# Performance work log

Measured on AMD Instinct MI355X. Metric: run time of the kernel, lower is better.

The kernel has to match this reference:

```python
import jax, jax.numpy as jnp
import numpy as np

B, DIM = 8192, 4096

def setup_inputs() -> dict:
    key = jax.random.key(0)
    k1, k2 = jax.random.split(key)
    a = jax.random.normal(k1, (B, 1, DIM), dtype=jnp.float32)
    b = jax.random.normal(k2, (B, 1, DIM), dtype=jnp.float32)
    return {"a": a, "b": b}

def reference(a, b):
    # Original layer builds a circulant matrix from b: row i is roll(b, shift=i),
    # i.e. C[i, k] = b[(k - i) % dim], then computes out[k] = sum_i a[i] * C[i, k]
    # = circular convolution of a and b. Equivalent (and O(d log d)) via FFT:
    d = a.shape[-1]
    fa = jnp.fft.rfft(a.astype(jnp.float32), axis=-1)
    fb = jnp.fft.rfft(b.astype(jnp.float32), axis=-1)
    out = jnp.fft.irfft(fa * fb, n=d, axis=-1)  # (B, 1, dim)
    return out.astype(a.dtype)
```

## Files before the change

kernel.cpp:

```cpp
#include <hip/hip_runtime.h>

#define FFT_N 4096
#define NT    256
#define SK(i) ((i) + ((i) >> 4))
#define PM(m) ((((m) & 3) << 2) | ((m) >> 2))

typedef float    cplx __attribute__((ext_vector_type(2)));
typedef _Float16 h4   __attribute__((ext_vector_type(4)));

__device__ __forceinline__ cplx mkc(float re, float im) { cplx c; c.x = re; c.y = im; return c; }
__device__ __forceinline__ h4 packh(cplx a, cplx b) {
    h4 v; v.x = (_Float16)a.x; v.y = (_Float16)a.y; v.z = (_Float16)b.x; v.w = (_Float16)b.y;
    return v;
}
__device__ __forceinline__ cplx cmul(cplx a, cplx b) {
    return mkc(a.x * b.x - a.y * b.y, a.x * b.y + a.y * b.x);
}
__device__ __forceinline__ cplx cmulc(cplx a, cplx b) {
    return mkc(a.x * b.x + a.y * b.y, a.y * b.x - a.x * b.y);
}

template <int SGN, bool PERMIN>
__device__ __forceinline__ void ip16(cplx* x) {
    const float S = (float)SGN;
    const float C1 = 0.92387953251128675613f;
    const float S1 = 0.38268343236508977173f;
    const float R2 = 0.70710678118654752440f;
#define BF4(i0, i1, i2, i3) do { \
        cplx x0 = x[i0], x1 = x[i1], x2 = x[i2], x3 = x[i3]; \
        cplx t0 = x0 + x2, t1 = x0 - x2; \
        cplx t2 = x1 + x3, t3 = x1 - x3; \
        cplx it3 = mkc(-S * t3.y, S * t3.x); \
        x[i0] = t0 + t2; x[i1] = t1 + it3; \
        x[i2] = t0 - t2; x[i3] = t1 - it3; \
    } while (0)
    if (!PERMIN) { BF4(0, 4, 8, 12); BF4(1, 5, 9, 13); BF4(2, 6, 10, 14); BF4(3, 7, 11, 15); }
    else         { BF4(0, 1, 2, 3);  BF4(4, 5, 6, 7);  BF4(8, 9, 10, 11); BF4(12, 13, 14, 15); }
    const cplx w1 = mkc(C1, S * S1), w2 = mkc(R2, S * R2), w3 = mkc(S1, S * C1);
    const cplx w6 = mkc(-R2, S * R2), w9 = mkc(-C1, -S * S1);
    x[5]  = cmul(x[5],  w1);
    x[6]  = cmul(x[6],  w2);
    x[7]  = cmul(x[7],  w3);
    x[9]  = cmul(x[9],  w2);
    { cplx v = x[10]; x[10] = mkc(-S * v.y, S * v.x); }
    x[11] = cmul(x[11], w6);
    x[13] = cmul(x[13], w3);
    x[14] = cmul(x[14], w6);
    x[15] = cmul(x[15], w9);
    if (!PERMIN) { BF4(0, 1, 2, 3);  BF4(4, 5, 6, 7);  BF4(8, 9, 10, 11); BF4(12, 13, 14, 15); }
    else         { BF4(0, 4, 8, 12); BF4(1, 5, 9, 13); BF4(2, 6, 10, 14); BF4(3, 7, 11, 15); }
#undef BF4
}

__global__ void twiddle_init(cplx* __restrict__ twA, cplx* __restrict__ twB) {
    int m = blockIdx.x * NT + threadIdx.x;
    if (m >= 4352) return;
    float s, c;
    if (m < 4096) {
        int r = m >> 8, t = m & 255;
        sincosf(-6.28318530717958647692f * (float)(t * r) / 4096.0f, &s, &c);
        twA[m] = mkc(c, s);
    } else {
        int k = m - 4096;
        int r = k >> 4, j = k & 15;
        sincosf(-6.28318530717958647692f * (float)(j * r) / 256.0f, &s, &c);
        twB[k] = mkc(c, s);
    }
}

__global__ __launch_bounds__(NT) void circconv4096_kernel(
    const float* __restrict__ A, const float* __restrict__ Bv,
    float* __restrict__ O,
    const cplx* __restrict__ twA, const cplx* __restrict__ twB)
{
    __shared__ h4 Z[SK(4095) + 1];
    const int t = threadIdx.x;
    const size_t r0 = (size_t)blockIdx.x * 2;
    const float* a0 = A + r0 * FFT_N;
    const float* b0 = Bv + r0 * FFT_N;
    const float* a1 = a0 + FFT_N;
    const float* b1 = b0 + FFT_N;
    float* o0 = O + r0 * FFT_N;
    float* o1 = o0 + FFT_N;

    cplx x0[16], x1[16];

#pragma unroll
    for (int q = 0; q < 16; ++q) { int g = t + 256 * q; x0[q] = mkc(a0[g], b0[g]); }
#pragma unroll
    for (int q = 0; q < 16; ++q) { int g = t + 256 * q; x1[q] = mkc(a1[g], b1[g]); }
    ip16<-1, false>(x0);
    ip16<-1, false>(x1);
#pragma unroll
    for (int m = 1; m < 16; ++m) {
        cplx w = twA[PM(m) * 256 + t];
        x0[m] = cmul(x0[m], w);
        x1[m] = cmul(x1[m], w);
    }
#pragma unroll
    for (int m = 0; m < 16; ++m) Z[SK(t + 256 * PM(m))] = packh(x0[m], x1[m]);
    __syncthreads();

    const int j = t & 15;
    const int base = ((t >> 4) << 8) + j;

#pragma unroll
    for (int q = 0; q < 16; ++q) {
        h4 v = Z[SK(base + 16 * q)];
        x0[q] = mkc((float)v.x, (float)v.y); x1[q] = mkc((float)v.z, (float)v.w);
    }
    ip16<-1, false>(x0);
    ip16<-1, false>(x1);
#pragma unroll
    for (int m = 1; m < 16; ++m) {
        cplx w = twB[PM(m) * 16 + j];
        x0[m] = cmul(x0[m], w);
        x1[m] = cmul(x1[m], w);
    }
    __builtin_amdgcn_wave_barrier();
#pragma unroll
    for (int m = 0; m < 16; ++m) Z[SK(base + 16 * PM(m))] = packh(x0[m], x1[m]);
    __builtin_amdgcn_wave_barrier();

    {
        const int b3 = t * 16;
        const float s = 1.0f / 8192.0f;
#pragma unroll
        for (int q = 0; q < 16; ++q) {
            h4 v = Z[SK(b3 + q)];
            x0[q] = mkc((float)v.x, (float)v.y); x1[q] = mkc((float)v.z, (float)v.w);
        }
        ip16<-1, false>(x0);
#pragma unroll
        for (int m = 0; m < 16; ++m) {
            cplx z = x0[m];
            x0[m] = mkc((z.x * z.x - z.y * z.y) * s, 2.0f * s * z.x * z.y);
        }
        ip16<1, true>(x0);
        ip16<-1, false>(x1);
#pragma unroll
        for (int m = 0; m < 16; ++m) {
            cplx z = x1[m];
            x1[m] = mkc((z.x * z.x - z.y * z.y) * s, 2.0f * s * z.x * z.y);
        }
        ip16<1, true>(x1);
        __builtin_amdgcn_wave_barrier();
#pragma unroll
        for (int q = 0; q < 16; ++q) Z[SK(b3 + q)] = packh(x0[q], x1[q]);
        __builtin_amdgcn_wave_barrier();
    }

#pragma unroll
    for (int r = 0; r < 16; ++r) {
        h4 v = Z[SK(base + 16 * r)];
        x0[r] = mkc((float)v.x, (float)v.y); x1[r] = mkc((float)v.z, (float)v.w);
    }
#pragma unroll
    for (int r = 1; r < 16; ++r) {
        cplx w = twB[r * 16 + j];
        x0[r] = cmulc(x0[r], w);
        x1[r] = cmulc(x1[r], w);
    }
    ip16<1, false>(x0);
    ip16<1, false>(x1);
    __builtin_amdgcn_wave_barrier();
#pragma unroll
    for (int m = 0; m < 16; ++m) Z[SK(base + 16 * PM(m))] = packh(x0[m], x1[m]);
    __syncthreads();

#pragma unroll
    for (int r = 0; r < 16; ++r) {
        h4 v = Z[SK(t + 256 * r)];
        x0[r] = mkc((float)v.x, (float)v.y); x1[r] = mkc((float)v.z, (float)v.w);
    }
#pragma unroll
    for (int r = 1; r < 16; ++r) {
        cplx w = twA[r * 256 + t];
        x0[r] = cmulc(x0[r], w);
        x1[r] = cmulc(x1[r], w);
    }
    ip16<1, false>(x0);
#pragma unroll
    for (int m = 0; m < 16; ++m) o0[t + 256 * PM(m)] = x0[m].y;
    ip16<1, false>(x1);
#pragma unroll
    for (int m = 0; m < 16; ++m) o1[t + 256 * PM(m)] = x1[m].y;
}

extern "C" void kernel_launch(void* const* d_in, const int* in_sizes, int n_in,
                              void* d_out, int out_size, void* d_ws, size_t ws_size,
                              hipStream_t stream) {
    const float* a = (const float*)d_in[0];
    const float* b = (const float*)d_in[1];
    float* out = (float*)d_out;
    cplx* twA = (cplx*)d_ws;
    cplx* twB = twA + 4096;
    const int B = in_sizes[0] / FFT_N;

    twiddle_init<<<17, NT, 0, stream>>>(twA, twB);
    circconv4096_kernel<<<B / 2, NT, 0, stream>>>(a, b, out, twA, twB);
}
```

Before: 119.7 us.

## Process several row pairs per block with software-prefetched next inputs

Each block now loops over four row pairs instead of one, and loads the next pair's inputs from global memory while the current pair's final inverse stage and output stores are still running. The aim is to hide global load latency behind compute and to amortize block launch and setup. The cost is a grid four times smaller (1024 blocks), an extra __syncthreads per iteration so shared memory can be reused, and possibly more register pressure from the prefetched values.

```diff
diff --git a/kernel.cpp b/kernel.cpp
--- a/kernel.cpp
+++ b/kernel.cpp
@@ -2,6 +2,7 @@
 
 #define FFT_N 4096
 #define NT    256
+#define PAIRS 4
 #define SK(i) ((i) + ((i) >> 4))
 #define PM(m) ((((m) & 3) << 2) | ((m) >> 2))
 
@@ -75,116 +76,132 @@
 {
     __shared__ h4 Z[SK(4095) + 1];
     const int t = threadIdx.x;
-    const size_t r0 = (size_t)blockIdx.x * 2;
-    const float* a0 = A + r0 * FFT_N;
-    const float* b0 = Bv + r0 * FFT_N;
-    const float* a1 = a0 + FFT_N;
-    const float* b1 = b0 + FFT_N;
-    float* o0 = O + r0 * FFT_N;
-    float* o1 = o0 + FFT_N;
-
-    cplx x0[16], x1[16];
-
-#pragma unroll
-    for (int q = 0; q < 16; ++q) { int g = t + 256 * q; x0[q] = mkc(a0[g], b0[g]); }
-#pragma unroll
-    for (int q = 0; q < 16; ++q) { int g = t + 256 * q; x1[q] = mkc(a1[g], b1[g]); }
-    ip16<-1, false>(x0);
-    ip16<-1, false>(x1);
-#pragma unroll
-    for (int m = 1; m < 16; ++m) {
-        cplx w = twA[PM(m) * 256 + t];
-        x0[m] = cmul(x0[m], w);
-        x1[m] = cmul(x1[m], w);
-    }
-#pragma unroll
-    for (int m = 0; m < 16; ++m) Z[SK(t + 256 * PM(m))] = packh(x0[m], x1[m]);
-    __syncthreads();
-
     const int j = t & 15;
     const int base = ((t >> 4) << 8) + j;
 
-#pragma unroll
-    for (int q = 0; q < 16; ++q) {
-        h4 v = Z[SK(base + 16 * q)];
-        x0[q] = mkc((float)v.x, (float)v.y); x1[q] = mkc((float)v.z, (float)v.w);
+    const size_t pair0 = (size_t)blockIdx.x * PAIRS;
+    const float* pa0 = A  + pair0 * 2 * FFT_N;
+    const float* pb0 = Bv + pair0 * 2 * FFT_N;
+    float*       po0 = O  + pair0 * 2 * FFT_N;
+
+    cplx x0[16], x1[16];
+
+#pragma unroll
+    for (int q = 0; q < 16; ++q) { int g = t + 256 * q; x0[q] = mkc(pa0[g], pb0[g]); }
+#pragma unroll
+    for (int q = 0; q < 16; ++q) { int g = t + 256 * q + FFT_N; x1[q] = mkc(pa0[g], pb0[g]); }
+
+#pragma unroll 1
+    for (int p = 0; p < PAIRS; ++p) {
+        ip16<-1, false>(x0);
+        ip16<-1, false>(x1);
+#pragma unroll
+        for (int m = 1; m < 16; ++m) {
+            cplx w = twA[PM(m) * 256 + t];
+            x0[m] = cmul(x0[m], w);
+            x1[m] = cmul(x1[m], w);
+        }
+#pragma unroll
+        for (int m = 0; m < 16; ++m) Z[SK(t + 256 * PM(m))] = packh(x0[m], x1[m]);
+        __syncthreads();
+
+#pragma unroll
+        for (int q = 0; q < 16; ++q) {
+            h4 v = Z[SK(base + 16 * q)];
+            x0[q] = mkc((float)v.x, (float)v.y); x1[q] = mkc((float)v.z, (float)v.w);
+        }
+        ip16<-1, false>(x0);
+        ip16<-1, false>(x1);
+#pragma unroll
+        for (int m = 1; m < 16; ++m) {
+            cplx w = twB[PM(m) * 16 + j];
+            x0[m] = cmul(x0[m], w);
+            x1[m] = cmul(x1[m], w);
+        }
+        __builtin_amdgcn_wave_barrier();
+#pragma unroll
+        for (int m = 0; m < 16; ++m) Z[SK(base + 16 * PM(m))] = packh(x0[m], x1[m]);
+        __builtin_amdgcn_wave_barrier();
+
+        {
+            const int b3 = t * 16;
+            const float s = 1.0f / 8192.0f;
+#pragma unroll
+            for (int q = 0; q < 16; ++q) {
+                h4 v = Z[SK(b3 + q)];
+                x0[q] = mkc((float)v.x, (float)v.y); x1[q] = mkc((float)v.z, (float)v.w);
+            }
+            ip16<-1, false>(x0);
+#pragma unroll
+            for (int m = 0; m < 16; ++m) {
+                cplx z = x0[m];
+                x0[m] = mkc((z.x * z.x - z.y * z.y) * s, 2.0f * s * z.x * z.y);
+            }
+            ip16<1, true>(x0);
+            ip16<-1, false>(x1);
+#pragma unroll
+            for (int m = 0; m < 16; ++m) {
+                cplx z = x1[m];
+                x1[m] = mkc((z.x * z.x - z.y * z.y) * s, 2.0f * s * z.x * z.y);
+            }
+            ip16<1, true>(x1);
+            __builtin_amdgcn_wave_barrier();
+#pragma unroll
+            for (int q = 0; q < 16; ++q) Z[SK(b3 + q)] = packh(x0[q], x1[q]);
+            __builtin_amdgcn_wave_barrier();
+        }
+
+#pragma unroll
+        for (int r = 0; r < 16; ++r) {
+            h4 v = Z[SK(base + 16 * r)];
+            x0[r] = mkc((float)v.x, (float)v.y); x1[r] = mkc((float)v.z, (float)v.w);
+        }
+#pragma unroll
+        for (int r = 1; r < 16; ++r) {
+            cplx w = twB[r * 16 + j];
+            x0[r] = cmulc(x0[r], w);
+            x1[r] = cmulc(x1[r], w);
+        }
+        ip16<1, false>(x0);
+        ip16<1, false>(x1);
+        __builtin_amdgcn_wave_barrier();
+#pragma unroll
+        for (int m = 0; m < 16; ++m) Z[SK(base + 16 * PM(m))] = packh(x0[m], x1[m]);
+        __syncthreads();
+
+#pragma unroll
+        for (int r = 0; r < 16; ++r) {
+            h4 v = Z[SK(t + 256 * r)];
+            x0[r] = mkc((float)v.x, (float)v.y); x1[r] = mkc((float)v.z, (float)v.w);
+        }
+        __syncthreads();
+
+#pragma unroll
+        for (int r = 1; r < 16; ++r) {
+            cplx w = twA[r * 256 + t];
+            x0[r] = cmulc(x0[r], w);
+            x1[r] = cmulc(x1[r], w);
+        }
+        ip16<1, false>(x0);
+#pragma unroll
+        for (int m = 0; m < 16; ++m) po0[t + 256 * PM(m)] = x0[m].y;
+        if (p + 1 < PAIRS) {
+            const float* na = pa0 + 2 * FFT_N;
+            const float* nb = pb0 + 2 * FFT_N;
+#pragma unroll
+            for (int q = 0; q < 16; ++q) { int g = t + 256 * q; x0[q] = mkc(na[g], nb[g]); }
+        }
+        ip16<1, false>(x1);
+#pragma unroll
+        for (int m = 0; m < 16; ++m) po0[t + 256 * PM(m) + FFT_N] = x1[m].y;
+        if (p + 1 < PAIRS) {
+            const float* na = pa0 + 2 * FFT_N;
+            const float* nb = pb0 + 2 * FFT_N;
+#pragma unroll
+            for (int q = 0; q < 16; ++q) { int g = t + 256 * q + FFT_N; x1[q] = mkc(na[g], nb[g]); }
+        }
+        pa0 += 2 * FFT_N; pb0 += 2 * FFT_N; po0 += 2 * FFT_N;
     }
-    ip16<-1, false>(x0);
-    ip16<-1, false>(x1);
-#pragma unroll
-    for (int m = 1; m < 16; ++m) {
-        cplx w = twB[PM(m) * 16 + j];
-        x0[m] = cmul(x0[m], w);
-        x1[m] = cmul(x1[m], w);
-    }
-    __builtin_amdgcn_wave_barrier();
-#pragma unroll
-    for (int m = 0; m < 16; ++m) Z[SK(base + 16 * PM(m))] = packh(x0[m], x1[m]);
-    __builtin_amdgcn_wave_barrier();
-
-    {
-        const int b3 = t * 16;
-        const float s = 1.0f / 8192.0f;
-#pragma unroll
-        for (int q = 0; q < 16; ++q) {
-            h4 v = Z[SK(b3 + q)];
-            x0[q] = mkc((float)v.x, (float)v.y); x1[q] = mkc((float)v.z, (float)v.w);
-        }
-        ip16<-1, false>(x0);
-#pragma unroll
-        for (int m = 0; m < 16; ++m) {
-            cplx z = x0[m];
-            x0[m] = mkc((z.x * z.x - z.y * z.y) * s, 2.0f * s * z.x * z.y);
-        }
-        ip16<1, true>(x0);
-        ip16<-1, false>(x1);
-#pragma unroll
-        for (int m = 0; m < 16; ++m) {
-            cplx z = x1[m];
-            x1[m] = mkc((z.x * z.x - z.y * z.y) * s, 2.0f * s * z.x * z.y);
-        }
-        ip16<1, true>(x1);
-        __builtin_amdgcn_wave_barrier();
-#pragma unroll
-        for (int q = 0; q < 16; ++q) Z[SK(b3 + q)] = packh(x0[q], x1[q]);
-        __builtin_amdgcn_wave_barrier();
-    }
-
-#pragma unroll
-    for (int r = 0; r < 16; ++r) {
-        h4 v = Z[SK(base + 16 * r)];
-        x0[r] = mkc((float)v.x, (float)v.y); x1[r] = mkc((float)v.z, (float)v.w);
-    }
-#pragma unroll
-    for (int r = 1; r < 16; ++r) {
-        cplx w = twB[r * 16 + j];
-        x0[r] = cmulc(x0[r], w);
-        x1[r] = cmulc(x1[r], w);
-    }
-    ip16<1, false>(x0);
-    ip16<1, false>(x1);
-    __builtin_amdgcn_wave_barrier();
-#pragma unroll
-    for (int m = 0; m < 16; ++m) Z[SK(base + 16 * PM(m))] = packh(x0[m], x1[m]);
-    __syncthreads();
-
-#pragma unroll
-    for (int r = 0; r < 16; ++r) {
-        h4 v = Z[SK(t + 256 * r)];
-        x0[r] = mkc((float)v.x, (float)v.y); x1[r] = mkc((float)v.z, (float)v.w);
-    }
-#pragma unroll
-    for (int r = 1; r < 16; ++r) {
-        cplx w = twA[r * 256 + t];
-        x0[r] = cmulc(x0[r], w);
-        x1[r] = cmulc(x1[r], w);
-    }
-    ip16<1, false>(x0);
-#pragma unroll
-    for (int m = 0; m < 16; ++m) o0[t + 256 * PM(m)] = x0[m].y;
-    ip16<1, false>(x1);
-#pragma unroll
-    for (int m = 0; m < 16; ++m) o1[t + 256 * PM(m)] = x1[m].y;
 }
 
 extern "C" void kernel_launch(void* const* d_in, const int* in_sizes, int n_in,
@@ -198,5 +215,5 @@
     const int B = in_sizes[0] / FFT_N;
 
     twiddle_init<<<17, NT, 0, stream>>>(twA, twB);
-    circconv4096_kernel<<<B / 2, NT, 0, stream>>>(a, b, out, twA, twB);
-}
+    circconv4096_kernel<<<B / (2 * PAIRS), NT, 0, stream>>>(a, b, out, twA, twB);
+}
```

Result: slower. 145.0 us (+21.1%).
